# Performance work log

Hardware: AMD Instinct MI355X
Metric: run time of the kernel (lower is better)

Reference implementation:

```python
import jax, jax.numpy as jnp
import numpy as np

FILTER_SIZE = 8
INPUT_DIM = 128
KERNEL_SIZE = 256


def setup_inputs() -> dict:
    key = jax.random.key(0)
    k1, k2, k3, k4 = jax.random.split(key, 4)
    user_batch = jax.random.normal(k1, (32, 2048, INPUT_DIM), dtype=jnp.float32)
    # Params initialized like torch.rand (uniform [0,1))
    filt = jax.random.uniform(k2, (FILTER_SIZE, INPUT_DIM), dtype=jnp.float32)
    W_k = jax.random.uniform(k3, (FILTER_SIZE * INPUT_DIM, KERNEL_SIZE), dtype=jnp.float32)
    b_k = jax.random.uniform(k4, (KERNEL_SIZE,), dtype=jnp.float32)
    return {"user_batch": user_batch, "filt": filt, "W_k": W_k, "b_k": b_k}


def reference(user_batch, filt, W_k, b_k):
    B, L, D = user_batch.shape
    F = filt.shape[0]
    n_win = L - F  # NOTE: original loop is range(0, L - F): exactly L - F windows
    # Gather sliding windows: [B, n_win, F, D]
    idx = jnp.arange(n_win)[:, None] + jnp.arange(F)[None, :]
    windows = user_batch[:, idx, :]
    # Elementwise mul with filter then contract flattened (F*D) against W_k
    W = W_k.reshape(F, D, -1)  # [F, D, K]
    out = jnp.einsum('blfd,fd,fdk->blk', windows, filt, W)
    return jax.nn.relu(out + b_k)
```

## Files before the change

kernel.cpp:

```cpp
#include <hip/hip_runtime.h>


#define L_SZ   2048
#define NWIN   2040
#define BM     128
#define MT     16

typedef __attribute__((ext_vector_type(8)))  short bf16x8;
typedef __attribute__((ext_vector_type(4)))  short bf16x4;
typedef __attribute__((ext_vector_type(16))) float f32x16;

static __device__ __forceinline__ short f2bf(float f) {
    union { float f; unsigned u; } v; v.f = f;
    unsigned r = v.u + 0x7FFFu + ((v.u >> 16) & 1u);
    return (short)(r >> 16);
}

static __device__ __forceinline__ void gload_lds16(const short* g, short* l) {
    __builtin_amdgcn_global_load_lds(
        (const __attribute__((address_space(1))) unsigned int*)g,
        (__attribute__((address_space(3))) unsigned int*)l, 16, 0, 0);
}

__global__ __launch_bounds__(256) void prep_w_kernel(
    const float* __restrict__ Wk, const float* __restrict__ filt,
    short* __restrict__ wp2)
{
    int g   = blockIdx.x * 256 + threadIdx.x;
    int R   = g >> 10;
    int w   = g & 1023;
    int np  = w >> 2;
    int pos = w & 3;
    int cs  = pos ^ ((np >> 1) & 3);
    int kb  = R * 32 + cs * 8;
    bf16x8 o;
    #pragma unroll
    for (int jj = 0; jj < 8; ++jj)
        o[jj] = f2bf(Wk[(size_t)(kb + jj) * 256 + np] * filt[kb + jj]);
    *reinterpret_cast<bf16x8*>(&wp2[(size_t)g * 8]) = o;
}

__global__ __launch_bounds__(512, 4) void cnn_enc_kernel(
    const float* __restrict__ ub, const short* __restrict__ wp2,
    const float* __restrict__ bk, float* __restrict__ out)
{
    __shared__ short sA[135 * 136];
    __shared__ short sB[2 * 8192];

    const int tid   = threadIdx.x;
    const int bid   = blockIdx.x;
    const int mt    = bid & 15;
    const int batch = bid >> 4;
    const int l0    = mt * BM;

    const int lane = tid & 63;
    const int wave = tid >> 6;
    const int wm   = wave >> 2;
    const int wn   = wave & 3;
    const int l32  = lane & 31;
    const int half = lane >> 5;

    auto stageB = [&](int c, int buf) {
        const short* wpb = wp2 + (size_t)c * 8192;
        #pragma unroll
        for (int r = 0; r < 2; ++r) {
            int ubase = r * 512 + wave * 64;
            gload_lds16(wpb + (ubase + lane) * 8, &sB[buf * 8192 + ubase * 8]);
        }
    };

    const float* ubb = ub + ((size_t)batch << 18);
    float4 av[9];
    #pragma unroll
    for (int u = 0; u < 9; ++u) {
        int idx = tid + u * 512;
        if (u < 8 || idx < 4320) {
            int r  = idx >> 5;
            int c4 = idx & 31;
            int rg = l0 + r; if (rg > L_SZ - 1) rg = L_SZ - 1;
            av[u] = *reinterpret_cast<const float4*>(
                ubb + ((size_t)rg << 7) + c4 * 4);
        }
    }
    asm volatile("" ::: "memory");
    stageB(0, 0);
    stageB(1, 1);
    asm volatile("" ::: "memory");
    #pragma unroll
    for (int u = 0; u < 9; ++u) {
        int idx = tid + u * 512;
        if (u < 8 || idx < 4320) {
            int r  = idx >> 5;
            int c4 = idx & 31;
            bf16x4 o;
            o.x = f2bf(av[u].x); o.y = f2bf(av[u].y);
            o.z = f2bf(av[u].z); o.w = f2bf(av[u].w);
            *reinterpret_cast<bf16x4*>(&sA[r * 136 + c4 * 4]) = o;
        }
    }

    f32x16 acc[2][2];
    #pragma unroll
    for (int i = 0; i < 2; ++i)
        #pragma unroll
        for (int j = 0; j < 2; ++j)
            acc[i][j] = (f32x16){0.f,0.f,0.f,0.f,0.f,0.f,0.f,0.f,
                                 0.f,0.f,0.f,0.f,0.f,0.f,0.f,0.f};

    int aoff[2];
    #pragma unroll
    for (int i = 0; i < 2; ++i)
        aoff[i] = (wm * 64 + i * 32 + l32) * 136 + half * 8;
    int bnp[2], bxor[2];
    #pragma unroll
    for (int j = 0; j < 2; ++j) {
        int np = wn * 64 + j * 32 + l32;
        bnp[j]  = np * 32;
        bxor[j] = (np >> 1) & 3;
    }

    asm volatile("s_waitcnt lgkmcnt(0)" ::: "memory");
    asm volatile("s_waitcnt vmcnt(2)" ::: "memory");
    __builtin_amdgcn_s_barrier();
    asm volatile("" ::: "memory");

    #pragma unroll 1
    for (int c = 0; c < 32; ++c) {
        const int f  = c >> 2, ds = c & 3;
        const int bb = (c & 1) * 8192;
        bf16x8 a[2][2], b[2][2];
        #pragma unroll
        for (int ks = 0; ks < 2; ++ks) {
            #pragma unroll
            for (int i = 0; i < 2; ++i)
                a[ks][i] = *reinterpret_cast<const bf16x8*>(
                    &sA[aoff[i] + f * 136 + ds * 32 + ks * 16]);
            #pragma unroll
            for (int j = 0; j < 2; ++j) {
                int c8 = ks * 2 + half;
                b[ks][j] = *reinterpret_cast<const bf16x8*>(
                    &sB[bb + bnp[j] + (c8 ^ bxor[j]) * 8]);
            }
        }
        if (c < 30) {
            asm volatile("s_waitcnt lgkmcnt(0)" ::: "memory");
            __builtin_amdgcn_s_barrier();
            asm volatile("" ::: "memory");
            stageB(c + 2, c & 1);
        }
        __builtin_amdgcn_s_setprio(1);
        #pragma unroll
        for (int ks = 0; ks < 2; ++ks)
            #pragma unroll
            for (int i = 0; i < 2; ++i)
                #pragma unroll
                for (int j = 0; j < 2; ++j)
                    acc[i][j] = __builtin_amdgcn_mfma_f32_32x32x16_bf16(
                        a[ks][i], b[ks][j], acc[i][j], 0, 0, 0);
        __builtin_amdgcn_s_setprio(0);
        if (c < 31) {
            if (c < 30) { asm volatile("s_waitcnt vmcnt(2)" ::: "memory"); }
            else        { asm volatile("s_waitcnt vmcnt(0)" ::: "memory"); }
            __builtin_amdgcn_s_barrier();
            asm volatile("" ::: "memory");
        }
    }

    #pragma unroll
    for (int j = 0; j < 2; ++j) {
        int n_glob = wn * 64 + j * 32 + l32;
        float bias = bk[n_glob];
        #pragma unroll
        for (int i = 0; i < 2; ++i) {
            #pragma unroll
            for (int r = 0; r < 16; ++r) {
                int row = (r & 3) + 8 * (r >> 2) + 4 * half;
                int l = l0 + wm * 64 + i * 32 + row;
                if (l < NWIN) {
                    float v = acc[i][j][r] + bias;
                    __builtin_nontemporal_store(
                        v > 0.f ? v : 0.f,
                        &out[((size_t)batch * NWIN + l) * 256 + n_glob]);
                }
            }
        }
    }
}

extern "C" void kernel_launch(void* const* d_in, const int* in_sizes, int n_in,
                              void* d_out, int out_size, void* d_ws, size_t ws_size,
                              hipStream_t stream) {
    const float* ub   = (const float*)d_in[0];
    const float* filt = (const float*)d_in[1];
    const float* Wk   = (const float*)d_in[2];
    const float* bk   = (const float*)d_in[3];
    float* out = (float*)d_out;
    short* wp2 = (short*)d_ws;

    hipLaunchKernelGGL(prep_w_kernel, dim3(128), dim3(256), 0, stream,
                       Wk, filt, wp2);
    hipLaunchKernelGGL(cnn_enc_kernel, dim3(32 * MT), dim3(512), 0, stream,
                       ub, wp2, bk, out);
}
```

Baseline: 124.9 us.

## Load weight fragments directly from global into registers, dropping LDS staging

Repacks the preprocessed weights into per-lane MFMA fragment order, so each lane can read its B operand straight from global memory (L2-resident) into registers. Register double-buffering replaces the LDS ring buffer and the per-step barriers. The goal is to cut LDS traffic and barrier stalls and to shrink shared memory, which may let more blocks fit per CU. In exchange, each wave fetches B separately from global/L2, which adds VMEM traffic, and load latency may not be fully hidden by a single step of MFMAs.

```diff
diff --git a/kernel.cpp b/kernel.cpp
--- a/kernel.cpp
+++ b/kernel.cpp
@@ -16,36 +16,29 @@
     return (short)(r >> 16);
 }
 
-static __device__ __forceinline__ void gload_lds16(const short* g, short* l) {
-    __builtin_amdgcn_global_load_lds(
-        (const __attribute__((address_space(1))) unsigned int*)g,
-        (__attribute__((address_space(3))) unsigned int*)l, 16, 0, 0);
-}
-
 __global__ __launch_bounds__(256) void prep_w_kernel(
     const float* __restrict__ Wk, const float* __restrict__ filt,
-    short* __restrict__ wp2)
+    short* __restrict__ wp3)
 {
     int g   = blockIdx.x * 256 + threadIdx.x;
-    int R   = g >> 10;
-    int w   = g & 1023;
-    int np  = w >> 2;
-    int pos = w & 3;
-    int cs  = pos ^ ((np >> 1) & 3);
-    int kb  = R * 32 + cs * 8;
+    int c   = g >> 10;
+    int nb  = (g >> 7) & 7;
+    int c8  = (g >> 5) & 3;
+    int l32 = g & 31;
+    int np  = nb * 32 + l32;
+    int kb  = c * 32 + c8 * 8;
     bf16x8 o;
     #pragma unroll
     for (int jj = 0; jj < 8; ++jj)
         o[jj] = f2bf(Wk[(size_t)(kb + jj) * 256 + np] * filt[kb + jj]);
-    *reinterpret_cast<bf16x8*>(&wp2[(size_t)g * 8]) = o;
+    *reinterpret_cast<bf16x8*>(&wp3[(size_t)g * 8]) = o;
 }
 
 __global__ __launch_bounds__(512, 4) void cnn_enc_kernel(
-    const float* __restrict__ ub, const short* __restrict__ wp2,
+    const float* __restrict__ ub, const short* __restrict__ wp3,
     const float* __restrict__ bk, float* __restrict__ out)
 {
     __shared__ short sA[135 * 136];
-    __shared__ short sB[2 * 8192];
 
     const int tid   = threadIdx.x;
     const int bid   = blockIdx.x;
@@ -60,15 +53,6 @@
     const int l32  = lane & 31;
     const int half = lane >> 5;
 
-    auto stageB = [&](int c, int buf) {
-        const short* wpb = wp2 + (size_t)c * 8192;
-        #pragma unroll
-        for (int r = 0; r < 2; ++r) {
-            int ubase = r * 512 + wave * 64;
-            gload_lds16(wpb + (ubase + lane) * 8, &sB[buf * 8192 + ubase * 8]);
-        }
-    };
-
     const float* ubb = ub + ((size_t)batch << 18);
     float4 av[9];
     #pragma unroll
@@ -82,10 +66,6 @@
                 ubb + ((size_t)rg << 7) + c4 * 4);
         }
     }
-    asm volatile("" ::: "memory");
-    stageB(0, 0);
-    stageB(1, 1);
-    asm volatile("" ::: "memory");
     #pragma unroll
     for (int u = 0; u < 9; ++u) {
         int idx = tid + u * 512;
@@ -111,43 +91,26 @@
     #pragma unroll
     for (int i = 0; i < 2; ++i)
         aoff[i] = (wm * 64 + i * 32 + l32) * 136 + half * 8;
-    int bnp[2], bxor[2];
-    #pragma unroll
-    for (int j = 0; j < 2; ++j) {
-        int np = wn * 64 + j * 32 + l32;
-        bnp[j]  = np * 32;
-        bxor[j] = (np >> 1) & 3;
-    }
 
-    asm volatile("s_waitcnt lgkmcnt(0)" ::: "memory");
-    asm volatile("s_waitcnt vmcnt(2)" ::: "memory");
-    __builtin_amdgcn_s_barrier();
-    asm volatile("" ::: "memory");
+    const short* wb = wp3 + (size_t)(wn * 2) * 1024 + (size_t)lane * 8;
+    auto loadB = [&](bf16x8 (&b)[2][2], int c) {
+        #pragma unroll
+        for (int ks = 0; ks < 2; ++ks)
+            #pragma unroll
+            for (int j = 0; j < 2; ++j)
+                b[ks][j] = *reinterpret_cast<const bf16x8*>(
+                    wb + (size_t)c * 8192 + j * 1024 + ks * 512);
+    };
 
-    #pragma unroll 1
-    for (int c = 0; c < 32; ++c) {
-        const int f  = c >> 2, ds = c & 3;
-        const int bb = (c & 1) * 8192;
-        bf16x8 a[2][2], b[2][2];
+    auto kstep = [&](int c, bf16x8 (&b)[2][2]) {
+        const int f = c >> 2, ds = c & 3;
+        bf16x8 a[2][2];
         #pragma unroll
-        for (int ks = 0; ks < 2; ++ks) {
+        for (int ks = 0; ks < 2; ++ks)
             #pragma unroll
             for (int i = 0; i < 2; ++i)
                 a[ks][i] = *reinterpret_cast<const bf16x8*>(
                     &sA[aoff[i] + f * 136 + ds * 32 + ks * 16]);
-            #pragma unroll
-            for (int j = 0; j < 2; ++j) {
-                int c8 = ks * 2 + half;
-                b[ks][j] = *reinterpret_cast<const bf16x8*>(
-                    &sB[bb + bnp[j] + (c8 ^ bxor[j]) * 8]);
-            }
-        }
-        if (c < 30) {
-            asm volatile("s_waitcnt lgkmcnt(0)" ::: "memory");
-            __builtin_amdgcn_s_barrier();
-            asm volatile("" ::: "memory");
-            stageB(c + 2, c & 1);
-        }
         __builtin_amdgcn_s_setprio(1);
         #pragma unroll
         for (int ks = 0; ks < 2; ++ks)
@@ -158,12 +121,18 @@
                     acc[i][j] = __builtin_amdgcn_mfma_f32_32x32x16_bf16(
                         a[ks][i], b[ks][j], acc[i][j], 0, 0, 0);
         __builtin_amdgcn_s_setprio(0);
-        if (c < 31) {
-            if (c < 30) { asm volatile("s_waitcnt vmcnt(2)" ::: "memory"); }
-            else        { asm volatile("s_waitcnt vmcnt(0)" ::: "memory"); }
-            __builtin_amdgcn_s_barrier();
-            asm volatile("" ::: "memory");
-        }
+    };
+
+    bf16x8 bA[2][2], bB[2][2];
+    loadB(bA, 0);
+    __syncthreads();
+
+    #pragma unroll 1
+    for (int c = 0; c < 32; c += 2) {
+        loadB(bB, c + 1);
+        kstep(c, bA);
+        if (c < 30) loadB(bA, c + 2);
+        kstep(c + 1, bB);
     }
 
     #pragma unroll
@@ -195,10 +164,10 @@
     const float* Wk   = (const float*)d_in[2];
     const float* bk   = (const float*)d_in[3];
     float* out = (float*)d_out;
-    short* wp2 = (short*)d_ws;
+    short* wp3 = (short*)d_ws;
 
     hipLaunchKernelGGL(prep_w_kernel, dim3(128), dim3(256), 0, stream,
-                       Wk, filt, wp2);
+                       Wk, filt, wp3);
     hipLaunchKernelGGL(cnn_enc_kernel, dim3(32 * MT), dim3(512), 0, stream,
-                       ub, wp2, bk, out);
+                       ub, wp3, bk, out);
 }
```

New measurement: 129.0 us. +3.3%, slower.

## Double the M tile to 256 rows with 1024-thread blocks and a 5-deep weight ring

Applied to the files above, without the earlier changes.

Each block now covers 256 sliding-window rows using 16 waves, halving the grid to 256 blocks. Each staged weight chunk is reused across twice as many rows, which halves weight reloads from L2. Weight chunks now stream through a 5-slot LDS ring, staged two chunks ahead, with one barrier per pair of chunks instead of per chunk, to cut synchronisation. The cost is about 152KB of LDS per block, so only one block fits per CU and latency hiding has less room.

```diff
diff --git a/kernel.cpp b/kernel.cpp
--- a/kernel.cpp
+++ b/kernel.cpp
@@ -3,8 +3,8 @@
 
 #define L_SZ   2048
 #define NWIN   2040
-#define BM     128
-#define MT     16
+#define BM     256
+#define MT     8
 
 typedef __attribute__((ext_vector_type(8)))  short bf16x8;
 typedef __attribute__((ext_vector_type(4)))  short bf16x4;
@@ -40,17 +40,17 @@
     *reinterpret_cast<bf16x8*>(&wp2[(size_t)g * 8]) = o;
 }
 
-__global__ __launch_bounds__(512, 4) void cnn_enc_kernel(
+__global__ __launch_bounds__(1024, 4) void cnn_enc_kernel(
     const float* __restrict__ ub, const short* __restrict__ wp2,
     const float* __restrict__ bk, float* __restrict__ out)
 {
-    __shared__ short sA[135 * 136];
-    __shared__ short sB[2 * 8192];
+    __shared__ short sA[263 * 136];
+    __shared__ short sB[5 * 8192];
 
     const int tid   = threadIdx.x;
     const int bid   = blockIdx.x;
-    const int mt    = bid & 15;
-    const int batch = bid >> 4;
+    const int mt    = bid & 7;
+    const int batch = bid >> 3;
     const int l0    = mt * BM;
 
     const int lane = tid & 63;
@@ -60,42 +60,37 @@
     const int l32  = lane & 31;
     const int half = lane >> 5;
 
-    auto stageB = [&](int c, int buf) {
-        const short* wpb = wp2 + (size_t)c * 8192;
-        #pragma unroll
-        for (int r = 0; r < 2; ++r) {
-            int ubase = r * 512 + wave * 64;
-            gload_lds16(wpb + (ubase + lane) * 8, &sB[buf * 8192 + ubase * 8]);
-        }
+    auto stageB = [&](int c) {
+        const short* src = wp2 + ((size_t)c * 1024 + tid) * 8;
+        gload_lds16(src, &sB[(c % 5) * 8192 + wave * 512]);
     };
 
     const float* ubb = ub + ((size_t)batch << 18);
-    float4 av[9];
-    #pragma unroll
-    for (int u = 0; u < 9; ++u) {
-        int idx = tid + u * 512;
-        if (u < 8 || idx < 4320) {
-            int r  = idx >> 5;
-            int c4 = idx & 31;
-            int rg = l0 + r; if (rg > L_SZ - 1) rg = L_SZ - 1;
-            av[u] = *reinterpret_cast<const float4*>(
-                ubb + ((size_t)rg << 7) + c4 * 4);
-        }
-    }
-    asm volatile("" ::: "memory");
-    stageB(0, 0);
-    stageB(1, 1);
-    asm volatile("" ::: "memory");
-    #pragma unroll
-    for (int u = 0; u < 9; ++u) {
-        int idx = tid + u * 512;
-        if (u < 8 || idx < 4320) {
-            int r  = idx >> 5;
-            int c4 = idx & 31;
-            bf16x4 o;
-            o.x = f2bf(av[u].x); o.y = f2bf(av[u].y);
-            o.z = f2bf(av[u].z); o.w = f2bf(av[u].w);
-            *reinterpret_cast<bf16x4*>(&sA[r * 136 + c4 * 4]) = o;
+    {
+        float4 av[9];
+        #pragma unroll
+        for (int u = 0; u < 9; ++u) {
+            int idx = tid + u * 1024;
+            if (u < 8 || idx < 8416) {
+                int r  = idx >> 5;
+                int c4 = idx & 31;
+                int rg = l0 + r; if (rg > L_SZ - 1) rg = L_SZ - 1;
+                av[u] = *reinterpret_cast<const float4*>(
+                    ubb + ((size_t)rg << 7) + c4 * 4);
+            }
+        }
+        stageB(0); stageB(1); stageB(2);
+        #pragma unroll
+        for (int u = 0; u < 9; ++u) {
+            int idx = tid + u * 1024;
+            if (u < 8 || idx < 8416) {
+                int r  = idx >> 5;
+                int c4 = idx & 31;
+                bf16x4 o;
+                o.x = f2bf(av[u].x); o.y = f2bf(av[u].y);
+                o.z = f2bf(av[u].z); o.w = f2bf(av[u].w);
+                *reinterpret_cast<bf16x4*>(&sA[r * 136 + c4 * 4]) = o;
+            }
         }
     }
 
@@ -119,15 +114,9 @@
         bxor[j] = (np >> 1) & 3;
     }
 
-    asm volatile("s_waitcnt lgkmcnt(0)" ::: "memory");
-    asm volatile("s_waitcnt vmcnt(2)" ::: "memory");
-    __builtin_amdgcn_s_barrier();
-    asm volatile("" ::: "memory");
-
-    #pragma unroll 1
-    for (int c = 0; c < 32; ++c) {
+    auto doChunk = [&](int c) {
         const int f  = c >> 2, ds = c & 3;
-        const int bb = (c & 1) * 8192;
+        const int bb = (c % 5) * 8192;
         bf16x8 a[2][2], b[2][2];
         #pragma unroll
         for (int ks = 0; ks < 2; ++ks) {
@@ -141,12 +130,6 @@
                 b[ks][j] = *reinterpret_cast<const bf16x8*>(
                     &sB[bb + bnp[j] + (c8 ^ bxor[j]) * 8]);
             }
-        }
-        if (c < 30) {
-            asm volatile("s_waitcnt lgkmcnt(0)" ::: "memory");
-            __builtin_amdgcn_s_barrier();
-            asm volatile("" ::: "memory");
-            stageB(c + 2, c & 1);
         }
         __builtin_amdgcn_s_setprio(1);
         #pragma unroll
@@ -158,11 +141,24 @@
                     acc[i][j] = __builtin_amdgcn_mfma_f32_32x32x16_bf16(
                         a[ks][i], b[ks][j], acc[i][j], 0, 0, 0);
         __builtin_amdgcn_s_setprio(0);
-        if (c < 31) {
-            if (c < 30) { asm volatile("s_waitcnt vmcnt(2)" ::: "memory"); }
+    };
+
+    asm volatile("s_waitcnt vmcnt(1) lgkmcnt(0)" ::: "memory");
+    __builtin_amdgcn_s_barrier();
+    __builtin_amdgcn_sched_barrier(0);
+
+    #pragma unroll 1
+    for (int p = 0; p < 16; ++p) {
+        const int c0 = 2 * p;
+        if (c0 + 3 < 32) stageB(c0 + 3);
+        if (c0 + 4 < 32) stageB(c0 + 4);
+        doChunk(c0);
+        doChunk(c0 + 1);
+        if (p < 15) {
+            if (p < 14) { asm volatile("s_waitcnt vmcnt(1)" ::: "memory"); }
             else        { asm volatile("s_waitcnt vmcnt(0)" ::: "memory"); }
             __builtin_amdgcn_s_barrier();
-            asm volatile("" ::: "memory");
+            __builtin_amdgcn_sched_barrier(0);
         }
     }
 
@@ -199,6 +195,6 @@
 
     hipLaunchKernelGGL(prep_w_kernel, dim3(128), dim3(256), 0, stream,
                        Wk, filt, wp2);
-    hipLaunchKernelGGL(cnn_enc_kernel, dim3(32 * MT), dim3(512), 0, stream,
+    hipLaunchKernelGGL(cnn_enc_kernel, dim3(32 * MT), dim3(1024), 0, stream,
                        ub, wp2, bk, out);
 }
```

New measurement: 123.4 us. No clear change (-1.2%).
